# Optimization experiments

Measured on AMD Instinct MI355X. Metric: run time of the kernel, lower is better.

Reference implementation:

```python
import jax, jax.numpy as jnp
import numpy as np

N_NODES = 50000
N_EDGES = 800000
IN_CH = 64
OUT_CH = 64
PRIOR_VAR = 1.0


def setup_inputs() -> dict:
    key = jax.random.key(0)
    ks = jax.random.split(key, 10)
    mean = jax.random.normal(ks[0], (N_NODES, IN_CH), dtype=jnp.float32)
    std = jax.random.uniform(ks[1], (N_NODES, IN_CH), dtype=jnp.float32)
    edge_index = jax.random.randint(ks[2], (2, N_EDGES), 0, N_NODES, dtype=jnp.int32)
    edge_weight = jax.random.uniform(ks[3], (N_EDGES,), dtype=jnp.float32)
    # Bayesian GCN parameters (xavier-ish mu, log_sigma init -3.0) for mean- and std-branches
    scale = float(np.sqrt(6.0 / (IN_CH + OUT_CH)))
    mu_mean = jax.random.uniform(ks[4], (IN_CH, OUT_CH), minval=-scale, maxval=scale, dtype=jnp.float32)
    log_sigma_mean = jnp.full((IN_CH, OUT_CH), -3.0, dtype=jnp.float32)
    mu_std = jax.random.uniform(ks[5], (IN_CH, OUT_CH), minval=-scale, maxval=scale, dtype=jnp.float32)
    log_sigma_std = jnp.full((IN_CH, OUT_CH), -3.0, dtype=jnp.float32)
    # reparameterization noise (drawn once so reference is deterministic)
    eps_mean = jax.random.normal(ks[6], (IN_CH, OUT_CH), dtype=jnp.float32)
    eps_std = jax.random.normal(ks[7], (IN_CH, OUT_CH), dtype=jnp.float32)
    return {
        "mean": mean, "std": std, "edge_index": edge_index, "edge_weight": edge_weight,
        "mu_mean": mu_mean, "log_sigma_mean": log_sigma_mean, "eps_mean": eps_mean,
        "mu_std": mu_std, "log_sigma_std": log_sigma_std, "eps_std": eps_std,
    }


def _gcn_propagate(x, weight, edge_index, edge_weight):
    # support = x @ W; then gather src rows, scale by edge_weight, scatter-add to dst
    support = jnp.matmul(x, weight)                      # [N, out]
    src, dst = edge_index[0], edge_index[1]
    msg = edge_weight[:, None] * support[src]            # [E, out]
    return jax.ops.segment_sum(msg, dst, num_segments=N_NODES)


def _kl(mu, log_sigma):
    pv = PRIOR_VAR
    kl = 0.5 * (jnp.exp(2.0 * log_sigma) / pv + mu ** 2 / pv
                - 2.0 * log_sigma - jnp.log(jnp.asarray(pv, mu.dtype)) - 1.0)
    return kl.sum()


def reference(mean, std, edge_index, edge_weight,
              mu_mean, log_sigma_mean, eps_mean,
              mu_std, log_sigma_std, eps_std):
    # mean branch
    w_mean = mu_mean + eps_mean * jnp.exp(log_sigma_mean)
    new_mean = _gcn_propagate(mean, w_mean, edge_index, edge_weight)
    kl_mean = _kl(mu_mean, log_sigma_mean)
    # std branch operates on variance with squared edge weights
    var = std ** 2
    w_std = mu_std + eps_std * jnp.exp(log_sigma_std)
    new_log_var = _gcn_propagate(var, w_std, edge_index, edge_weight ** 2)
    kl_std = _kl(mu_std, log_sigma_std)
    new_std = jnp.sqrt(jnp.exp(new_log_var) + 1e-6)
    total_kl = kl_mean + kl_std
    return (new_mean, new_std, total_kl)
```

## Files before the change

### kernel.cpp

```cpp
#include <hip/hip_runtime.h>

#define N_NODES 50000
#define N_EDGES 800000
#define CH 64
#define OUT_OFF_STD (N_NODES * CH)
#define OUT_OFF_KL  (2 * N_NODES * CH)
#define CAP 64

__device__ __forceinline__ float rl_f(float v, int lane) {
    return __uint_as_float(
        (unsigned)__builtin_amdgcn_readlane(__float_as_int(v), lane));
}
__device__ __forceinline__ int rl_i(unsigned v, int lane) {
    return __builtin_amdgcn_readlane((int)v, lane);
}
__device__ __forceinline__ unsigned f2bf(float f) {
    unsigned u = __float_as_uint(f);
    return (u + 0x7fffu + ((u >> 16) & 1u)) >> 16;
}

__global__ __launch_bounds__(256) void gemfill_kernel(
    const float* __restrict__ mean, const float* __restrict__ stdv,
    const float* __restrict__ mu_m, const float* __restrict__ ls_m,
    const float* __restrict__ eps_m,
    const float* __restrict__ mu_s, const float* __restrict__ ls_s,
    const float* __restrict__ eps_s,
    const int* __restrict__ ei, const float* __restrict__ ew,
    int* __restrict__ cur, uint2* __restrict__ bins,
    unsigned* __restrict__ sup, float* __restrict__ kl_out)
{
    __shared__ float Wt_m[64 * 68];
    __shared__ float Wt_v[64 * 68];

    const int tid = threadIdx.x;

    if (blockIdx.x & 1) {
        int e = (blockIdx.x >> 1) * 256 + tid;
        int src = ei[e];
        int dst = ei[N_EDGES + e];
        float w = ew[e];
        int slot = atomicAdd(&cur[dst], 1);
        if (slot < CAP)
            bins[(size_t)dst * CAP + slot] =
                make_uint2((unsigned)src, __float_as_uint(w));
        if (blockIdx.x == 1) {
            float kl = 0.0f;
            for (int i = tid; i < CH * CH; i += 256) {
                float mu = mu_m[i], ls = ls_m[i];
                kl += 0.5f * (expf(2.0f * ls) + mu * mu - 2.0f * ls - 1.0f);
                mu = mu_s[i]; ls = ls_s[i];
                kl += 0.5f * (expf(2.0f * ls) + mu * mu - 2.0f * ls - 1.0f);
            }
            for (int off = 32; off > 0; off >>= 1)
                kl += __shfl_down(kl, off, 64);
            if ((tid & 63) == 0) Wt_m[tid >> 6] = kl;
            __syncthreads();
            if (tid == 0)
                kl_out[0] = Wt_m[0] + Wt_m[1] + Wt_m[2] + Wt_m[3];
        }
        return;
    }

    for (int i = tid; i < CH * CH; i += 256) {
        int k = i >> 6, c = i & 63;
        Wt_m[c * 68 + k] = mu_m[i] + eps_m[i] * expf(ls_m[i]);
        Wt_v[c * 68 + k] = mu_s[i] + eps_s[i] * expf(ls_s[i]);
    }

    const int wave = tid >> 6, col = tid & 63;
    const int row0 = (blockIdx.x >> 1) * 16 + wave * 4;

    float xm0 = mean[(size_t)(row0 + 0) * CH + col];
    float xm1 = mean[(size_t)(row0 + 1) * CH + col];
    float xm2 = mean[(size_t)(row0 + 2) * CH + col];
    float xm3 = mean[(size_t)(row0 + 3) * CH + col];
    float t0 = stdv[(size_t)(row0 + 0) * CH + col];
    float t1 = stdv[(size_t)(row0 + 1) * CH + col];
    float t2 = stdv[(size_t)(row0 + 2) * CH + col];
    float t3 = stdv[(size_t)(row0 + 3) * CH + col];
    float xs0 = t0 * t0, xs1 = t1 * t1, xs2 = t2 * t2, xs3 = t3 * t3;

    __syncthreads();

    float am0 = 0, am1 = 0, am2 = 0, am3 = 0;
    float av0 = 0, av1 = 0, av2 = 0, av3 = 0;
#pragma unroll
    for (int k4 = 0; k4 < 16; ++k4) {
        float4 wm = *(const float4*)&Wt_m[col * 68 + k4 * 4];
        float4 wv = *(const float4*)&Wt_v[col * 68 + k4 * 4];
#pragma unroll
        for (int t = 0; t < 4; ++t) {
            const int k = k4 * 4 + t;
            const float wmt = (&wm.x)[t];
            const float wvt = (&wv.x)[t];
            am0 += rl_f(xm0, k) * wmt;
            am1 += rl_f(xm1, k) * wmt;
            am2 += rl_f(xm2, k) * wmt;
            am3 += rl_f(xm3, k) * wmt;
            av0 += rl_f(xs0, k) * wvt;
            av1 += rl_f(xs1, k) * wvt;
            av2 += rl_f(xs2, k) * wvt;
            av3 += rl_f(xs3, k) * wvt;
        }
    }

    size_t rb = (size_t)row0 * CH + col;
    sup[rb + 0 * CH] = f2bf(am0) | (f2bf(av0) << 16);
    sup[rb + 1 * CH] = f2bf(am1) | (f2bf(av1) << 16);
    sup[rb + 2 * CH] = f2bf(am2) | (f2bf(av2) << 16);
    sup[rb + 3 * CH] = f2bf(am3) | (f2bf(av3) << 16);
}

__global__ __launch_bounds__(256) void gather_kernel(
    const int* __restrict__ cur, const uint2* __restrict__ bins,
    const unsigned* __restrict__ sup, float* __restrict__ out)
{
    const int wave = threadIdx.x >> 6;
    const int col = threadIdx.x & 63;
    const int n = blockIdx.x * 4 + wave;

    int cnt = cur[n];
    if (cnt > CAP) cnt = CAP;
    uint2 p = make_uint2(0u, 0u);
    if (col < cnt) p = bins[(size_t)n * CAP + col];

    float accM = 0.0f, accV = 0.0f;
    for (int i = 0; i < cnt; i += 4) {
        const bool v1 = (i + 1 < cnt), v2 = (i + 2 < cnt), v3 = (i + 3 < cnt);
        int s0 = rl_i(p.x, i);
        int s1 = v1 ? rl_i(p.x, i + 1) : 0;
        int s2 = v2 ? rl_i(p.x, i + 2) : 0;
        int s3 = v3 ? rl_i(p.x, i + 3) : 0;
        float w0 = __uint_as_float((unsigned)rl_i(p.y, i));
        float w1 = v1 ? __uint_as_float((unsigned)rl_i(p.y, i + 1)) : 0.0f;
        float w2 = v2 ? __uint_as_float((unsigned)rl_i(p.y, i + 2)) : 0.0f;
        float w3 = v3 ? __uint_as_float((unsigned)rl_i(p.y, i + 3)) : 0.0f;
        unsigned q0 = sup[(size_t)s0 * CH + col];
        unsigned q1 = sup[(size_t)s1 * CH + col];
        unsigned q2 = sup[(size_t)s2 * CH + col];
        unsigned q3 = sup[(size_t)s3 * CH + col];
        float m0 = __uint_as_float(q0 << 16), vv0 = __uint_as_float(q0 & 0xFFFF0000u);
        float m1 = __uint_as_float(q1 << 16), vv1 = __uint_as_float(q1 & 0xFFFF0000u);
        float m2 = __uint_as_float(q2 << 16), vv2 = __uint_as_float(q2 & 0xFFFF0000u);
        float m3 = __uint_as_float(q3 << 16), vv3 = __uint_as_float(q3 & 0xFFFF0000u);
        accM += w0 * m0 + w1 * m1;
        accM += w2 * m2 + w3 * m3;
        accV += (w0 * w0) * vv0 + (w1 * w1) * vv1;
        accV += (w2 * w2) * vv2 + (w3 * w3) * vv3;
    }
    out[(size_t)n * CH + col] = accM;
    out[OUT_OFF_STD + (size_t)n * CH + col] = sqrtf(expf(accV) + 1e-6f);
}

extern "C" void kernel_launch(void* const* d_in, const int* in_sizes, int n_in,
                              void* d_out, int out_size, void* d_ws, size_t ws_size,
                              hipStream_t stream)
{
    const float* mean  = (const float*)d_in[0];
    const float* stdv  = (const float*)d_in[1];
    const int*   ei    = (const int*)d_in[2];
    const float* ew    = (const float*)d_in[3];
    const float* mu_m  = (const float*)d_in[4];
    const float* ls_m  = (const float*)d_in[5];
    const float* eps_m = (const float*)d_in[6];
    const float* mu_s  = (const float*)d_in[7];
    const float* ls_s  = (const float*)d_in[8];
    const float* eps_s = (const float*)d_in[9];

    float* out = (float*)d_out;
    float* ws  = (float*)d_ws;
    int*      cur  = (int*)ws;
    unsigned* sup  = (unsigned*)(ws + 50000);
    uint2*    bins = (uint2*)(ws + 50000 + 6400000);

    sup  = (unsigned*)(cur + N_NODES);
    bins = (uint2*)(sup + (size_t)N_NODES * CH);

    hipMemsetAsync(cur, 0, N_NODES * sizeof(int), stream);

    gemfill_kernel<<<6250, 256, 0, stream>>>(mean, stdv,
                                             mu_m, ls_m, eps_m,
                                             mu_s, ls_s, eps_s,
                                             ei, ew, cur, bins, sup,
                                             out + OUT_OFF_KL);
    gather_kernel<<<N_NODES / 4, 256, 0, stream>>>(cur, bins, sup, out);
}
```

Baseline: 211.7 us.

## Use bf16 MFMA for node-feature GEMM with prepacked weight fragments

```diff
diff --git a/kernel.cpp b/kernel.cpp
--- a/kernel.cpp
+++ b/kernel.cpp
@@ -6,11 +6,12 @@
 #define OUT_OFF_STD (N_NODES * CH)
 #define OUT_OFF_KL  (2 * N_NODES * CH)
 #define CAP 64
-
-__device__ __forceinline__ float rl_f(float v, int lane) {
-    return __uint_as_float(
-        (unsigned)__builtin_amdgcn_readlane(__float_as_int(v), lane));
-}
+#define GEMM_BLOCKS 782
+#define FILL_BLOCKS 3125
+
+typedef __attribute__((ext_vector_type(8))) short short8;
+typedef __attribute__((ext_vector_type(4))) float f32x4;
+
 __device__ __forceinline__ int rl_i(unsigned v, int lane) {
     return __builtin_amdgcn_readlane((int)v, lane);
 }
@@ -19,23 +20,48 @@
     return (u + 0x7fffu + ((u >> 16) & 1u)) >> 16;
 }
 
-__global__ __launch_bounds__(256) void gemfill_kernel(
-    const float* __restrict__ mean, const float* __restrict__ stdv,
+__global__ __launch_bounds__(256) void wkl_kernel(
     const float* __restrict__ mu_m, const float* __restrict__ ls_m,
     const float* __restrict__ eps_m,
     const float* __restrict__ mu_s, const float* __restrict__ ls_s,
     const float* __restrict__ eps_s,
+    unsigned short* __restrict__ fragBm, unsigned short* __restrict__ fragBv,
+    float* __restrict__ kl_out)
+{
+    float kl = 0.0f;
+    for (int f = threadIdx.x; f < CH * CH; f += 256) {
+        int j = f & 7, l = (f >> 3) & 63, ch = f >> 9;
+        int k = (ch & 1) * 32 + ((l >> 4) & 3) * 8 + j;
+        int n = (ch >> 1) * 16 + (l & 15);
+        int idx = k * CH + n;
+        float mu = mu_m[idx], ls = ls_m[idx];
+        fragBm[f] = (unsigned short)f2bf(mu + eps_m[idx] * expf(ls));
+        kl += 0.5f * (expf(2.0f * ls) + mu * mu - 2.0f * ls - 1.0f);
+        mu = mu_s[idx]; ls = ls_s[idx];
+        fragBv[f] = (unsigned short)f2bf(mu + eps_s[idx] * expf(ls));
+        kl += 0.5f * (expf(2.0f * ls) + mu * mu - 2.0f * ls - 1.0f);
+    }
+    for (int off = 32; off > 0; off >>= 1)
+        kl += __shfl_down(kl, off, 64);
+    __shared__ float red[4];
+    if ((threadIdx.x & 63) == 0) red[threadIdx.x >> 6] = kl;
+    __syncthreads();
+    if (threadIdx.x == 0)
+        kl_out[0] = red[0] + red[1] + red[2] + red[3];
+}
+
+__global__ __launch_bounds__(256) void gemfill_kernel(
+    const float* __restrict__ mean, const float* __restrict__ stdv,
+    const unsigned short* __restrict__ fragBm,
+    const unsigned short* __restrict__ fragBv,
     const int* __restrict__ ei, const float* __restrict__ ew,
     int* __restrict__ cur, uint2* __restrict__ bins,
-    unsigned* __restrict__ sup, float* __restrict__ kl_out)
-{
-    __shared__ float Wt_m[64 * 68];
-    __shared__ float Wt_v[64 * 68];
-
+    unsigned* __restrict__ sup)
+{
     const int tid = threadIdx.x;
 
-    if (blockIdx.x & 1) {
-        int e = (blockIdx.x >> 1) * 256 + tid;
+    if (blockIdx.x >= GEMM_BLOCKS) {
+        int e = (blockIdx.x - GEMM_BLOCKS) * 256 + tid;
         int src = ei[e];
         int dst = ei[N_EDGES + e];
         float w = ew[e];
@@ -43,72 +69,62 @@
         if (slot < CAP)
             bins[(size_t)dst * CAP + slot] =
                 make_uint2((unsigned)src, __float_as_uint(w));
-        if (blockIdx.x == 1) {
-            float kl = 0.0f;
-            for (int i = tid; i < CH * CH; i += 256) {
-                float mu = mu_m[i], ls = ls_m[i];
-                kl += 0.5f * (expf(2.0f * ls) + mu * mu - 2.0f * ls - 1.0f);
-                mu = mu_s[i]; ls = ls_s[i];
-                kl += 0.5f * (expf(2.0f * ls) + mu * mu - 2.0f * ls - 1.0f);
-            }
-            for (int off = 32; off > 0; off >>= 1)
-                kl += __shfl_down(kl, off, 64);
-            if ((tid & 63) == 0) Wt_m[tid >> 6] = kl;
-            __syncthreads();
-            if (tid == 0)
-                kl_out[0] = Wt_m[0] + Wt_m[1] + Wt_m[2] + Wt_m[3];
+        return;
+    }
+
+    const int lane = tid & 63, wave = tid >> 6;
+    const int row0 = blockIdx.x * 64 + wave * 16;
+    if (row0 >= N_NODES) return;
+
+    const int m = lane & 15;
+    const int q = (lane >> 4) & 3;
+    const float* mrow = mean + (size_t)(row0 + m) * CH + q * 8;
+    const float* srow = stdv + (size_t)(row0 + m) * CH + q * 8;
+
+    short8 aM[2], aV[2];
+#pragma unroll
+    for (int h = 0; h < 2; ++h) {
+        float4 x0 = *(const float4*)(mrow + h * 32);
+        float4 x1 = *(const float4*)(mrow + h * 32 + 4);
+        float4 s0 = *(const float4*)(srow + h * 32);
+        float4 s1 = *(const float4*)(srow + h * 32 + 4);
+        aM[h][0] = (short)f2bf(x0.x); aM[h][1] = (short)f2bf(x0.y);
+        aM[h][2] = (short)f2bf(x0.z); aM[h][3] = (short)f2bf(x0.w);
+        aM[h][4] = (short)f2bf(x1.x); aM[h][5] = (short)f2bf(x1.y);
+        aM[h][6] = (short)f2bf(x1.z); aM[h][7] = (short)f2bf(x1.w);
+        aV[h][0] = (short)f2bf(s0.x * s0.x); aV[h][1] = (short)f2bf(s0.y * s0.y);
+        aV[h][2] = (short)f2bf(s0.z * s0.z); aV[h][3] = (short)f2bf(s0.w * s0.w);
+        aV[h][4] = (short)f2bf(s1.x * s1.x); aV[h][5] = (short)f2bf(s1.y * s1.y);
+        aV[h][6] = (short)f2bf(s1.z * s1.z); aV[h][7] = (short)f2bf(s1.w * s1.w);
+    }
+
+    f32x4 accM[4], accV[4];
+#pragma unroll
+    for (int c = 0; c < 4; ++c) {
+        accM[c] = (f32x4)0.0f;
+        accV[c] = (f32x4)0.0f;
+    }
+#pragma unroll
+    for (int c = 0; c < 4; ++c) {
+#pragma unroll
+        for (int h = 0; h < 2; ++h) {
+            short8 bm = *(const short8*)(fragBm + ((c * 2 + h) * 64 + lane) * 8);
+            short8 bv = *(const short8*)(fragBv + ((c * 2 + h) * 64 + lane) * 8);
+            accM[c] = __builtin_amdgcn_mfma_f32_16x16x32_bf16(aM[h], bm, accM[c], 0, 0, 0);
+            accV[c] = __builtin_amdgcn_mfma_f32_16x16x32_bf16(aV[h], bv, accV[c], 0, 0, 0);
         }
-        return;
-    }
-
-    for (int i = tid; i < CH * CH; i += 256) {
-        int k = i >> 6, c = i & 63;
-        Wt_m[c * 68 + k] = mu_m[i] + eps_m[i] * expf(ls_m[i]);
-        Wt_v[c * 68 + k] = mu_s[i] + eps_s[i] * expf(ls_s[i]);
-    }
-
-    const int wave = tid >> 6, col = tid & 63;
-    const int row0 = (blockIdx.x >> 1) * 16 + wave * 4;
-
-    float xm0 = mean[(size_t)(row0 + 0) * CH + col];
-    float xm1 = mean[(size_t)(row0 + 1) * CH + col];
-    float xm2 = mean[(size_t)(row0 + 2) * CH + col];
-    float xm3 = mean[(size_t)(row0 + 3) * CH + col];
-    float t0 = stdv[(size_t)(row0 + 0) * CH + col];
-    float t1 = stdv[(size_t)(row0 + 1) * CH + col];
-    float t2 = stdv[(size_t)(row0 + 2) * CH + col];
-    float t3 = stdv[(size_t)(row0 + 3) * CH + col];
-    float xs0 = t0 * t0, xs1 = t1 * t1, xs2 = t2 * t2, xs3 = t3 * t3;
-
-    __syncthreads();
-
-    float am0 = 0, am1 = 0, am2 = 0, am3 = 0;
-    float av0 = 0, av1 = 0, av2 = 0, av3 = 0;
-#pragma unroll
-    for (int k4 = 0; k4 < 16; ++k4) {
-        float4 wm = *(const float4*)&Wt_m[col * 68 + k4 * 4];
-        float4 wv = *(const float4*)&Wt_v[col * 68 + k4 * 4];
-#pragma unroll
-        for (int t = 0; t < 4; ++t) {
-            const int k = k4 * 4 + t;
-            const float wmt = (&wm.x)[t];
-            const float wvt = (&wv.x)[t];
-            am0 += rl_f(xm0, k) * wmt;
-            am1 += rl_f(xm1, k) * wmt;
-            am2 += rl_f(xm2, k) * wmt;
-            am3 += rl_f(xm3, k) * wmt;
-            av0 += rl_f(xs0, k) * wvt;
-            av1 += rl_f(xs1, k) * wvt;
-            av2 += rl_f(xs2, k) * wvt;
-            av3 += rl_f(xs3, k) * wvt;
+    }
+
+    const int rg = lane >> 4;
+#pragma unroll
+    for (int c = 0; c < 4; ++c) {
+#pragma unroll
+        for (int r = 0; r < 4; ++r) {
+            int node = row0 + rg * 4 + r;
+            sup[(size_t)node * CH + c * 16 + m] =
+                f2bf(accM[c][r]) | (f2bf(accV[c][r]) << 16);
         }
     }
-
-    size_t rb = (size_t)row0 * CH + col;
-    sup[rb + 0 * CH] = f2bf(am0) | (f2bf(av0) << 16);
-    sup[rb + 1 * CH] = f2bf(am1) | (f2bf(av1) << 16);
-    sup[rb + 2 * CH] = f2bf(am2) | (f2bf(av2) << 16);
-    sup[rb + 3 * CH] = f2bf(am3) | (f2bf(av3) << 16);
 }
 
 __global__ __launch_bounds__(256) void gather_kernel(
@@ -168,20 +184,17 @@
     const float* eps_s = (const float*)d_in[9];
 
     float* out = (float*)d_out;
-    float* ws  = (float*)d_ws;
-    int*      cur  = (int*)ws;
-    unsigned* sup  = (unsigned*)(ws + 50000);
-    uint2*    bins = (uint2*)(ws + 50000 + 6400000);
-
-    sup  = (unsigned*)(cur + N_NODES);
-    bins = (uint2*)(sup + (size_t)N_NODES * CH);
+    int*            cur    = (int*)d_ws;
+    unsigned*       sup    = (unsigned*)(cur + N_NODES);
+    uint2*          bins   = (uint2*)(sup + (size_t)N_NODES * CH);
+    unsigned short* fragBm = (unsigned short*)(bins + (size_t)N_NODES * CAP);
+    unsigned short* fragBv = fragBm + CH * CH;
 
     hipMemsetAsync(cur, 0, N_NODES * sizeof(int), stream);
 
-    gemfill_kernel<<<6250, 256, 0, stream>>>(mean, stdv,
-                                             mu_m, ls_m, eps_m,
-                                             mu_s, ls_s, eps_s,
-                                             ei, ew, cur, bins, sup,
-                                             out + OUT_OFF_KL);
+    wkl_kernel<<<1, 256, 0, stream>>>(mu_m, ls_m, eps_m, mu_s, ls_s, eps_s,
+                                      fragBm, fragBv, out + OUT_OFF_KL);
+    gemfill_kernel<<<GEMM_BLOCKS + FILL_BLOCKS, 256, 0, stream>>>(
+        mean, stdv, fragBm, fragBv, ei, ew, cur, bins, sup);
     gather_kernel<<<N_NODES / 4, 256, 0, stream>>>(cur, bins, sup, out);
 }
```

New measurement: 205.3 us. 3.0% less time.
